# Optimization experiments

Hardware: AMD Instinct MI355X
Metric: run time of the kernel (lower is better)

Reference implementation:

```python
import jax, jax.numpy as jnp
import numpy as np

B, S, D, H, NUM_REL = 8, 1024, 1024, 16, 512
HD = D // H  # head size = 64


def setup_inputs() -> dict:
    key = jax.random.key(0)
    ks = jax.random.split(key, 12)
    sc = 0.02  # weight init scale for numerical stability
    inp = {
        "query": jax.random.normal(ks[0], (B, S, D), jnp.float32),
        "key": jax.random.normal(ks[1], (B, S, D), jnp.float32),
        "value": jax.random.normal(ks[2], (B, S, D), jnp.float32),
        "Wq": jax.random.normal(ks[3], (D, D), jnp.float32) * sc,
        "bq": jnp.zeros((D,), jnp.float32),
        "Wk": jax.random.normal(ks[4], (D, D), jnp.float32) * sc,
        "bk": jnp.zeros((D,), jnp.float32),
        "Wv": jax.random.normal(ks[5], (D, D), jnp.float32) * sc,
        "bv": jnp.zeros((D,), jnp.float32),
        "Wo": jax.random.normal(ks[6], (D, D), jnp.float32) * sc,
        "bo": jnp.zeros((D,), jnp.float32),
        "pos_table": jax.random.normal(ks[7], (NUM_REL, HD), jnp.float32) * sc,
        # True = masked position (causal: cannot attend to future)
        "mask": jnp.broadcast_to(jnp.triu(jnp.ones((S, S), bool), k=1), (B, S, S)),
    }
    return inp


def reference(query, key, value, Wq, bq, Wk, bk, Wv, bv, Wo, bo, pos_table, mask):
    Bq, Sq, Dm = query.shape
    hd = Dm // H

    def proj(x, W, b):
        # nn.Linear: x @ W.T + b, then split heads -> [B, H, S, hd]
        return (x @ W.T + b).reshape(Bq, Sq, H, hd).transpose(0, 2, 1, 3)

    q = proj(query, Wq, bq)
    k = proj(key, Wk, bk)
    v = proj(value, Wv, bv)

    scores = jnp.einsum("bhid,bhjd->bhij", q, k)

    # relative-position bias: idxs[i,j] = clip(i - j, 0, NUM_REL-1)
    t = jnp.arange(Sq)
    idxs = jnp.clip(t[:, None] - t[None, :], 0, pos_table.shape[0] - 1)
    pos = pos_table[idxs]  # [S, S, hd]
    scores = scores + jnp.einsum("bhid,ijd->bhij", q, pos)

    scores = scores / np.sqrt(hd).astype(np.float32)
    scores = jnp.where(mask[:, None, :, :], jnp.float32(-1e9), scores)
    prob = jax.nn.softmax(scores, axis=-1)  # dropout p=0.0 -> identity

    out = jnp.einsum("bhij,bhjd->bhid", prob, v)
    out = out.transpose(0, 2, 1, 3).reshape(Bq, Sq, Dm)
    return out @ Wo.T + bo
```

## Files before the change

kernel.cpp:

```cpp
#include <hip/hip_runtime.h>
#include <stdint.h>

#define DEV __device__ __forceinline__

typedef unsigned short u16;
typedef __bf16 bf16x8 __attribute__((ext_vector_type(8)));
typedef float  f32x4  __attribute__((ext_vector_type(4)));
typedef unsigned short u16x8 __attribute__((ext_vector_type(8)));
typedef unsigned short u16x4 __attribute__((ext_vector_type(4)));
typedef float  fvec4  __attribute__((ext_vector_type(4)));

constexpr int Sz   = 1024;
constexpr int Dm   = 1024;
constexpr int HDm  = 64;
constexpr int NREL = 512;
constexpr int Mrows = 8192;
constexpr int KV   = 32;

DEV u16 f2bf(float f) { return __builtin_bit_cast(u16, (__bf16)f); }
DEV float bf2f(u16 h) { return __builtin_bit_cast(float, (uint32_t)h << 16); }
DEV f32x4 mfma16(bf16x8 a, bf16x8 b, f32x4 c) {
  return __builtin_amdgcn_mfma_f32_16x16x32_bf16(a, b, c, 0, 0, 0);
}
DEV float ex2(float x) {
  float r;
  asm("v_exp_f32 %0, %1" : "=v"(r) : "v"(x));
  return r;
}

DEV u16x4 tr0(const u16* p) {
  u16x4 d;
  asm volatile("ds_read_b64_tr_b16 %0, %1"
               : "=v"(d)
               : "v"((const __attribute__((address_space(3))) u16*)p));
  return d;
}
DEV u16x4 tr512(const u16* p) {
  u16x4 d;
  asm volatile("ds_read_b64_tr_b16 %0, %1 offset:512"
               : "=v"(d)
               : "v"((const __attribute__((address_space(3))) u16*)p));
  return d;
}
DEV bf16x8 mk8(u16x4 a, u16x4 b) {
  u16x8 r;
  r[0] = a[0]; r[1] = a[1]; r[2] = a[2]; r[3] = a[3];
  r[4] = b[0]; r[5] = b[1]; r[6] = b[2]; r[7] = b[3];
  return __builtin_bit_cast(bf16x8, r);
}
DEV void gload(const u16* src, u16* dst) {
  __builtin_amdgcn_global_load_lds(
      (const __attribute__((address_space(1))) void*)src,
      (__attribute__((address_space(3))) void*)dst, 16, 0, 0);
}

__global__ __launch_bounds__(256) void cvt_kernel(const float* __restrict__ in,
                                                  u16* __restrict__ out) {
  size_t i = (size_t)blockIdx.x * 256 + threadIdx.x;
  fvec4 v = *(const fvec4*)(in + i * 4);
  u16x4 o;
  o[0] = f2bf(v[0]); o[1] = f2bf(v[1]); o[2] = f2bf(v[2]); o[3] = f2bf(v[3]);
  *(u16x4*)(out + i * 4) = o;
}

__global__ __launch_bounds__(256) void cvt3_kernel(const float* __restrict__ a,
                                                   const float* __restrict__ b,
                                                   const float* __restrict__ c,
                                                   u16* __restrict__ oa,
                                                   u16* __restrict__ ob,
                                                   u16* __restrict__ oc) {
  const int bid = blockIdx.x;
  const int seg = bid >> 13;
  const float* in = seg == 0 ? a : seg == 1 ? b : c;
  u16* out = seg == 0 ? oa : seg == 1 ? ob : oc;
  size_t i = (size_t)(bid & 8191) * 256 + threadIdx.x;
  fvec4 v = *(const fvec4*)(in + i * 4);
  u16x4 o;
  o[0] = f2bf(v[0]); o[1] = f2bf(v[1]); o[2] = f2bf(v[2]); o[3] = f2bf(v[3]);
  *(u16x4*)(out + i * 4) = o;
}

template<bool OUT_BF16>
DEV void gemm_body(const u16* __restrict__ A, const u16* __restrict__ Bw,
                   const float* __restrict__ bias, void* __restrict__ Cout,
                   int m0, int n0, u16* As, u16* Bs) {
  const int tid = threadIdx.x;
  const int wave = tid >> 6, lane = tid & 63;
  const int lr = lane & 15, lg = lane >> 4;
  const int wr = (wave >> 1) * 64, wc = (wave & 1) * 64;

  auto issue = [&](int t) {
    const int k0 = t * 64;
    u16* Ad = As + (t & 1) * (128 * 64);
    u16* Bd = Bs + (t & 1) * (128 * 64);
    #pragma unroll
    for (int it = 0; it < 4; ++it) {
      int chunk = it * 256 + tid;
      int row = chunk >> 3, c16 = chunk & 7;
      gload(Bw + (size_t)(n0 + row) * Dm + k0 + ((c16 ^ (row & 7)) * 8),
            Bd + (it * 256 + wave * 64) * 8);
      gload(A + (size_t)(m0 + row) * Dm + k0 + ((c16 ^ (row & 7)) * 8),
            Ad + (it * 256 + wave * 64) * 8);
    }
  };

  issue(0);
  f32x4 acc[4][4] = {};
  for (int t = 0; t < 16; ++t) {
    if (t < 15) {
      issue(t + 1);
      asm volatile("s_waitcnt vmcnt(8)" ::: "memory");
    } else {
      asm volatile("s_waitcnt vmcnt(0)" ::: "memory");
    }
    __builtin_amdgcn_s_barrier();
    const u16* Ab = As + (t & 1) * (128 * 64);
    const u16* Bb = Bs + (t & 1) * (128 * 64);
    #pragma unroll
    for (int kk = 0; kk < 2; ++kk) {
      bf16x8 af[4], bf_[4];
      #pragma unroll
      for (int m = 0; m < 4; ++m)
        af[m] = *(const bf16x8*)&Ab[(wr + m * 16 + lr) * 64 + (((kk * 4 + lg) ^ (lr & 7)) * 8)];
      #pragma unroll
      for (int n = 0; n < 4; ++n)
        bf_[n] = *(const bf16x8*)&Bb[(wc + n * 16 + lr) * 64 + (((kk * 4 + lg) ^ (lr & 7)) * 8)];
      __builtin_amdgcn_s_setprio(1);
      #pragma unroll
      for (int m = 0; m < 4; ++m)
        #pragma unroll
        for (int n = 0; n < 4; ++n)
          acc[m][n] = mfma16(af[m], bf_[n], acc[m][n]);
      __builtin_amdgcn_s_setprio(0);
    }
    __builtin_amdgcn_s_barrier();
  }

  float bv[4];
  #pragma unroll
  for (int n = 0; n < 4; ++n) bv[n] = bias[n0 + wc + n * 16 + lr];
  #pragma unroll
  for (int m = 0; m < 4; ++m) {
    #pragma unroll
    for (int n = 0; n < 4; ++n) {
      const int gcol = n0 + wc + n * 16 + lr;
      #pragma unroll
      for (int r = 0; r < 4; ++r) {
        const int grow = m0 + wr + m * 16 + lg * 4 + r;
        float v = acc[m][n][r] + bv[n];
        if (OUT_BF16)
          ((u16*)Cout)[(size_t)grow * Dm + gcol] = f2bf(v);
        else
          ((float*)Cout)[(size_t)grow * Dm + gcol] = v;
      }
    }
  }
}

template<bool OUT_BF16>
__global__ __launch_bounds__(256) void gemm1_kernel(const u16* __restrict__ A,
                                                    const u16* __restrict__ Bw,
                                                    const float* __restrict__ bias,
                                                    void* __restrict__ Cout) {
  __shared__ u16 As[2 * 128 * 64];
  __shared__ u16 Bs[2 * 128 * 64];
  const int r = blockIdx.x;
  const int xcd = r & 7, loc = r >> 3;
  const int m0 = (xcd * 8 + (loc & 7)) * 128;
  const int n0 = (loc >> 3) * 128;
  gemm_body<OUT_BF16>(A, Bw, bias, Cout, m0, n0, As, Bs);
}

__global__ __launch_bounds__(256) void gemm3_kernel(
    const u16* __restrict__ Xq, const u16* __restrict__ Xk, const u16* __restrict__ Xv,
    const u16* __restrict__ Wq, const u16* __restrict__ Wk, const u16* __restrict__ Wv,
    const float* __restrict__ bq, const float* __restrict__ bk, const float* __restrict__ bv,
    u16* __restrict__ Cq, u16* __restrict__ Ck, u16* __restrict__ Cv) {
  __shared__ u16 As[2 * 128 * 64];
  __shared__ u16 Bs[2 * 128 * 64];
  const int flat = blockIdx.x;
  const int seg = flat >> 9;
  const int r = flat & 511;
  const int xcd = r & 7, loc = r >> 3;
  const int m0 = (xcd * 8 + (loc & 7)) * 128;
  const int n0 = (loc >> 3) * 128;
  const u16* A = seg == 0 ? Xq : seg == 1 ? Xk : Xv;
  const u16* Bw = seg == 0 ? Wq : seg == 1 ? Wk : Wv;
  const float* bias = seg == 0 ? bq : seg == 1 ? bk : bv;
  u16* C = seg == 0 ? Cq : seg == 1 ? Ck : Cv;
  gemm_body<true>(A, Bw, bias, C, m0, n0, As, Bs);
}

__global__ __launch_bounds__(256, 4) void attn_kernel(const u16* __restrict__ Q,
                                                      const u16* __restrict__ Kb,
                                                      const u16* __restrict__ Vb,
                                                      const u16* __restrict__ posB,
                                                      u16* __restrict__ O) {
  __shared__ u16 Ks[2][KV * 64];
  __shared__ u16 Vs[2][KV * 64];
  __shared__ u16 ring[128 * 64];
  __shared__ u16 SH[4][16 * 40];

  const int tid = threadIdx.x;
  const int wave = tid >> 6, lane = tid & 63;
  const int lr = lane & 15, lg = lane >> 4;
  const int bid = blockIdx.x;
  const int xcd = bid & 7;
  const int idx = bid >> 3;
  const int bhl = idx & 15;
  const int pp_ = idx >> 4;
  const int bh  = xcd * 16 + bhl;
  const int b = bh >> 4, h = bh & 15;

  u16* SHW = SH[wave];
  const size_t rowbase = (size_t)(b * Sz) * Dm + h * HDm;

  const int krow = tid >> 3, kc = tid & 7;
  const int vj = ((tid >> 5) << 2) | ((tid >> 1) & 3);
  const int vd = ((tid >> 3) & 3) * 16 + (tid & 1) * 8;
  const int rrow = tid >> 3, rcol = tid & 7;

  auto issueKV = [&](int t) {
    const int j0 = t * KV;
    const int bsel = t & 1;
    gload(Kb + rowbase + (size_t)(j0 + krow) * Dm + ((kc ^ (krow & 7)) * 8),
          &Ks[bsel][wave * 512]);
    gload(Vb + rowbase + (size_t)(j0 + vj) * Dm + vd, &Vs[bsel][wave * 512]);
  };
  auto stageRing = [&](int cb) {
    const int rel = cb + rrow;
    const int slot = rel & 127;
    const int cl = rel < 0 ? 0 : (rel > NREL - 1 ? NREL - 1 : rel);
    gload(posB + cl * 64 + ((rcol ^ (slot & 7)) * 8),
          &ring[((cb & 127) + wave * 8) * 64]);
  };

  constexpr float SC = 0.125f * 1.44269504f;

  for (int job = 0; job < 2; ++job) {
    const int qi = job ? pp_ : 15 - pp_;
    const int qb = qi * 64;
    const int wq = qb + wave * 16;
    const int nt = 2 * qi + 2;
    const int qg = wq + lr;

    const u16* qptr = Q + rowbase + (size_t)(wq + lr) * Dm;
    bf16x8 qf[2];
    qf[0] = *(const bf16x8*)(qptr + lg * 8);
    qf[1] = *(const bf16x8*)(qptr + 32 + lg * 8);

    float b511;
    {
      const u16* pp = posB + (NREL - 1) * HDm;
      bf16x8 pa0 = *(const bf16x8*)(pp + lg * 8);
      bf16x8 pa1 = *(const bf16x8*)(pp + 32 + lg * 8);
      f32x4 a = {};
      a = mfma16(pa0, qf[0], a);
      a = mfma16(pa1, qf[1], a);
      b511 = a[0];
    }

    stageRing(qb + 32);
    stageRing(qb);
    stageRing(qb - 32);
    issueKV(0);

    f32x4 oacc[4] = {};
    float m_i = -1e30f, l_i = 0.f;

    for (int t = 0; t < nt; ++t) {
      const int j0 = t * KV;
      const int bsel = t & 1;
      const bool active = (j0 <= wq + 15);
      const bool clamp = (wq - j0 - 31) >= NREL - 1;
      const int wb = wq - j0 - 31;

      if (t + 1 < nt) {
        stageRing(qb - 32 * (t + 1) - 32);
        issueKV(t + 1);
        asm volatile("s_waitcnt vmcnt(3)" ::: "memory");
      } else {
        asm volatile("s_waitcnt vmcnt(0)" ::: "memory");
      }
      __builtin_amdgcn_s_barrier();

      if (active) {
        if (!clamp) {
          #pragma unroll
          for (int wg = 0; wg < 3; ++wg) {
            const int rrel = wb + wg * 16 + lr;
            const int slot = rrel & 127;
            const u16* rp = &ring[slot * 64];
            f32x4 a = {};
            a = mfma16(qf[0], *(const bf16x8*)&rp[((0 + lg) ^ (slot & 7)) * 8], a);
            a = mfma16(qf[1], *(const bf16x8*)&rp[((4 + lg) ^ (slot & 7)) * 8], a);
            #pragma unroll
            for (int r = 0; r < 4; ++r) {
              const int q = lg * 4 + r;
              const int col = q - (wg * 16 + lr) + 31;
              if (col >= 0 && col < 32)
                SHW[q * 40 + col] = f2bf(a[r]);
            }
          }
        }

        __builtin_amdgcn_s_setprio(1);
        f32x4 s0 = {}, s1 = {};
        const u16* KT = &Ks[bsel][0];
        s0 = mfma16(*(const bf16x8*)&KT[(0 + lr) * 64 + (((0 + lg) ^ (lr & 7)) * 8)], qf[0], s0);
        s0 = mfma16(*(const bf16x8*)&KT[(0 + lr) * 64 + (((4 + lg) ^ (lr & 7)) * 8)], qf[1], s0);
        s1 = mfma16(*(const bf16x8*)&KT[(16 + lr) * 64 + (((0 + lg) ^ (lr & 7)) * 8)], qf[0], s1);
        s1 = mfma16(*(const bf16x8*)&KT[(16 + lr) * 64 + (((4 + lg) ^ (lr & 7)) * 8)], qf[1], s1);
        __builtin_amdgcn_s_setprio(0);

        float p0[4], p1[4];
        float tmax = -3e38f;
        if (clamp) {
          #pragma unroll
          for (int r = 0; r < 4; ++r) {
            p0[r] = (s0[r] + b511) * SC; tmax = fmaxf(tmax, p0[r]);
            p1[r] = (s1[r] + b511) * SC; tmax = fmaxf(tmax, p1[r]);
          }
        } else {
          u16x4 bv0 = *(const u16x4*)&SHW[lr * 40 + lg * 4];
          u16x4 bv1 = *(const u16x4*)&SHW[lr * 40 + 16 + lg * 4];
          #pragma unroll
          for (int r = 0; r < 4; ++r) {
            float v0 = (s0[r] + bf2f(bv0[r])) * SC;
            if (j0 + lg * 4 + r > qg) v0 = -1e9f;
            p0[r] = v0; tmax = fmaxf(tmax, v0);
            float v1 = (s1[r] + bf2f(bv1[r])) * SC;
            if (j0 + 16 + lg * 4 + r > qg) v1 = -1e9f;
            p1[r] = v1; tmax = fmaxf(tmax, v1);
          }
        }
        tmax = fmaxf(tmax, __shfl_xor(tmax, 16));
        tmax = fmaxf(tmax, __shfl_xor(tmax, 32));

        if (!__all(tmax <= m_i + 11.5f)) {
          float mn = fmaxf(m_i, tmax);
          float sc = ex2(m_i - mn);
          m_i = mn; l_i *= sc;
          #pragma unroll
          for (int dg = 0; dg < 4; ++dg) oacc[dg] *= sc;
        }

        float lsum = 0.f;
        #pragma unroll
        for (int r = 0; r < 4; ++r) {
          p0[r] = ex2(p0[r] - m_i); lsum += p0[r];
          p1[r] = ex2(p1[r] - m_i); lsum += p1[r];
        }
        lsum += __shfl_xor(lsum, 16);
        lsum += __shfl_xor(lsum, 32);
        l_i += lsum;

        u16x4 pk0, pk1;
        #pragma unroll
        for (int r = 0; r < 4; ++r) { pk0[r] = f2bf(p0[r]); pk1[r] = f2bf(p1[r]); }
        *(u16x4*)&SHW[lr * 40 + lg * 4] = pk0;
        *(u16x4*)&SHW[lr * 40 + 16 + lg * 4] = pk1;

        bf16x8 pB = *(const bf16x8*)&SHW[lr * 40 + lg * 8];

        u16x4 va[4][2];
        #pragma unroll
        for (int dg = 0; dg < 4; ++dg) {
          const u16* base = &Vs[bsel][(2 * lg) * 256 + dg * 64 + lr * 4];
          va[dg][0] = tr0(base);
          va[dg][1] = tr512(base);
        }
        asm volatile("s_waitcnt lgkmcnt(0)" ::: "memory");
        __builtin_amdgcn_sched_barrier(0);
        __builtin_amdgcn_s_setprio(1);
        #pragma unroll
        for (int dg = 0; dg < 4; ++dg)
          oacc[dg] = mfma16(mk8(va[dg][0], va[dg][1]), pB, oacc[dg]);
        __builtin_amdgcn_s_setprio(0);
      }
      __builtin_amdgcn_s_barrier();
    }

    const float inv = 1.0f / l_i;
    const size_t obase = rowbase + (size_t)qg * Dm;
    #pragma unroll
    for (int dg = 0; dg < 4; ++dg) {
      u16x4 w;
      #pragma unroll
      for (int r = 0; r < 4; ++r) w[r] = f2bf(oacc[dg][r] * inv);
      *(u16x4*)&O[obase + dg * 16 + lg * 4] = w;
    }
  }
}

extern "C" void kernel_launch(void* const* d_in, const int* in_sizes, int n_in,
                              void* d_out, int out_size, void* d_ws, size_t ws_size,
                              hipStream_t stream) {
  const float* query = (const float*)d_in[0];
  const float* key   = (const float*)d_in[1];
  const float* value = (const float*)d_in[2];
  const float* Wq    = (const float*)d_in[3];
  const float* bq    = (const float*)d_in[4];
  const float* Wk    = (const float*)d_in[5];
  const float* bk    = (const float*)d_in[6];
  const float* Wv    = (const float*)d_in[7];
  const float* bv    = (const float*)d_in[8];
  const float* Wo    = (const float*)d_in[9];
  const float* bo    = (const float*)d_in[10];
  const float* pos   = (const float*)d_in[11];

  char* ws = (char*)d_ws;
  u16* WqB  = (u16*)(ws);
  u16* WkB  = (u16*)(ws + (2ull << 20));
  u16* WvB  = (u16*)(ws + (4ull << 20));
  u16* WoB  = (u16*)(ws + (6ull << 20));
  u16* posB = (u16*)(ws + (8ull << 20));
  u16* Xq   = (u16*)(ws + (9ull << 20));
  u16* Xk   = (u16*)(ws + (25ull << 20));
  u16* Xv   = (u16*)(ws + (41ull << 20));
  u16* Qb   = (u16*)(ws + (57ull << 20));
  u16* Kb   = (u16*)(ws + (73ull << 20));
  u16* Ob   = Xq;

  const bool bigws = ws_size >= (105ull << 20);
  u16* Vb = bigws ? (u16*)(ws + (89ull << 20)) : Xk;

  cvt_kernel<<<1024, 256, 0, stream>>>(Wq, WqB);
  cvt_kernel<<<1024, 256, 0, stream>>>(Wk, WkB);
  cvt_kernel<<<1024, 256, 0, stream>>>(Wv, WvB);
  cvt_kernel<<<1024, 256, 0, stream>>>(Wo, WoB);
  cvt_kernel<<<32,   256, 0, stream>>>(pos, posB);
  cvt3_kernel<<<24576, 256, 0, stream>>>(query, key, value, Xq, Xk, Xv);

  if (bigws) {
    gemm3_kernel<<<1536, 256, 0, stream>>>(Xq, Xk, Xv, WqB, WkB, WvB,
                                           bq, bk, bv, Qb, Kb, Vb);
  } else {
    gemm1_kernel<true><<<512, 256, 0, stream>>>(Xq, WqB, bq, Qb);
    gemm1_kernel<true><<<512, 256, 0, stream>>>(Xk, WkB, bk, Kb);
    gemm1_kernel<true><<<512, 256, 0, stream>>>(Xv, WvB, bv, Vb);
  }

  attn_kernel<<<1024, 256, 0, stream>>>(Qb, Kb, Vb, posB, Ob);

  gemm1_kernel<false><<<512, 256, 0, stream>>>(Ob, WoB, bo, d_out);
}
```

Measured before the change: 192.2 us.

## Fuse fp32-to-bf16 activation conversion into QKV GEMM and merge weight casts

The QKV projection GEMM now reads fp32 activations directly. It loads them into registers, converts them to bf16 and writes them to swizzled LDS, which removes the separate cvt3 pass that wrote and re-read 48MB of bf16 copies. The five small weight and pos-table conversion launches are merged into one kernel. The GEMM epilogue is changed to emit vectorized 4-wide stores by swapping the MFMA operand order, so each lane holds contiguous columns. In exchange, the fp32 A path waits on vmcnt(0) every iteration, and its register-staged prefetch may pipeline less deeply than the previous direct global-to-LDS double buffer.

```diff
diff --git a/kernel.cpp b/kernel.cpp
--- a/kernel.cpp
+++ b/kernel.cpp
@@ -54,36 +54,85 @@
       (__attribute__((address_space(3))) void*)dst, 16, 0, 0);
 }
 
-__global__ __launch_bounds__(256) void cvt_kernel(const float* __restrict__ in,
-                                                  u16* __restrict__ out) {
-  size_t i = (size_t)blockIdx.x * 256 + threadIdx.x;
+__global__ __launch_bounds__(256) void cvtw_kernel(const float* __restrict__ w0,
+                                                   const float* __restrict__ w1,
+                                                   const float* __restrict__ w2,
+                                                   const float* __restrict__ w3,
+                                                   const float* __restrict__ ps,
+                                                   u16* __restrict__ o0,
+                                                   u16* __restrict__ o1,
+                                                   u16* __restrict__ o2,
+                                                   u16* __restrict__ o3,
+                                                   u16* __restrict__ op) {
+  const int bid = blockIdx.x;
+  const float* in;
+  u16* out;
+  int local;
+  if (bid < 4096) {
+    const int s = bid >> 10;
+    in = s == 0 ? w0 : s == 1 ? w1 : s == 2 ? w2 : w3;
+    out = s == 0 ? o0 : s == 1 ? o1 : s == 2 ? o2 : o3;
+    local = bid & 1023;
+  } else {
+    in = ps; out = op; local = bid - 4096;
+  }
+  size_t i = (size_t)local * 256 + threadIdx.x;
   fvec4 v = *(const fvec4*)(in + i * 4);
   u16x4 o;
   o[0] = f2bf(v[0]); o[1] = f2bf(v[1]); o[2] = f2bf(v[2]); o[3] = f2bf(v[3]);
   *(u16x4*)(out + i * 4) = o;
 }
 
-__global__ __launch_bounds__(256) void cvt3_kernel(const float* __restrict__ a,
-                                                   const float* __restrict__ b,
-                                                   const float* __restrict__ c,
-                                                   u16* __restrict__ oa,
-                                                   u16* __restrict__ ob,
-                                                   u16* __restrict__ oc) {
-  const int bid = blockIdx.x;
-  const int seg = bid >> 13;
-  const float* in = seg == 0 ? a : seg == 1 ? b : c;
-  u16* out = seg == 0 ? oa : seg == 1 ? ob : oc;
-  size_t i = (size_t)(bid & 8191) * 256 + threadIdx.x;
-  fvec4 v = *(const fvec4*)(in + i * 4);
-  u16x4 o;
-  o[0] = f2bf(v[0]); o[1] = f2bf(v[1]); o[2] = f2bf(v[2]); o[3] = f2bf(v[3]);
-  *(u16x4*)(out + i * 4) = o;
-}
-
 template<bool OUT_BF16>
-DEV void gemm_body(const u16* __restrict__ A, const u16* __restrict__ Bw,
-                   const float* __restrict__ bias, void* __restrict__ Cout,
-                   int m0, int n0, u16* As, u16* Bs) {
+DEV void gemm_epilogue(const float* bias, void* Cout, int m0, int n0,
+                       int wr, int wc, int lr, int lg, f32x4 acc[4][4]) {
+  #pragma unroll
+  for (int m = 0; m < 4; ++m) {
+    const int grow = m0 + wr + m * 16 + lr;
+    #pragma unroll
+    for (int n = 0; n < 4; ++n) {
+      const int gcol = n0 + wc + n * 16 + lg * 4;
+      fvec4 bb = *(const fvec4*)&bias[gcol];
+      if (OUT_BF16) {
+        u16x4 w;
+        #pragma unroll
+        for (int r = 0; r < 4; ++r) w[r] = f2bf(acc[m][n][r] + bb[r]);
+        *(u16x4*)&((u16*)Cout)[(size_t)grow * Dm + gcol] = w;
+      } else {
+        fvec4 w;
+        #pragma unroll
+        for (int r = 0; r < 4; ++r) w[r] = acc[m][n][r] + bb[r];
+        *(fvec4*)&((float*)Cout)[(size_t)grow * Dm + gcol] = w;
+      }
+    }
+  }
+}
+
+DEV void gemm_compute(const u16* Ab, const u16* Bb, int wr, int wc,
+                      int lr, int lg, f32x4 acc[4][4]) {
+  #pragma unroll
+  for (int kk = 0; kk < 2; ++kk) {
+    bf16x8 af[4], bf_[4];
+    #pragma unroll
+    for (int m = 0; m < 4; ++m)
+      af[m] = *(const bf16x8*)&Ab[(wr + m * 16 + lr) * 64 + (((kk * 4 + lg) ^ (lr & 7)) * 8)];
+    #pragma unroll
+    for (int n = 0; n < 4; ++n)
+      bf_[n] = *(const bf16x8*)&Bb[(wc + n * 16 + lr) * 64 + (((kk * 4 + lg) ^ (lr & 7)) * 8)];
+    __builtin_amdgcn_s_setprio(1);
+    #pragma unroll
+    for (int m = 0; m < 4; ++m)
+      #pragma unroll
+      for (int n = 0; n < 4; ++n)
+        acc[m][n] = mfma16(bf_[n], af[m], acc[m][n]);
+    __builtin_amdgcn_s_setprio(0);
+  }
+}
+
+template<bool OUT_BF16>
+DEV void gemm_body16(const u16* __restrict__ A, const u16* __restrict__ Bw,
+                     const float* __restrict__ bias, void* __restrict__ Cout,
+                     int m0, int n0, u16* As, u16* Bs) {
   const int tid = threadIdx.x;
   const int wave = tid >> 6, lane = tid & 63;
   const int lr = lane & 15, lg = lane >> 4;
@@ -114,47 +163,70 @@
       asm volatile("s_waitcnt vmcnt(0)" ::: "memory");
     }
     __builtin_amdgcn_s_barrier();
-    const u16* Ab = As + (t & 1) * (128 * 64);
-    const u16* Bb = Bs + (t & 1) * (128 * 64);
-    #pragma unroll
-    for (int kk = 0; kk < 2; ++kk) {
-      bf16x8 af[4], bf_[4];
-      #pragma unroll
-      for (int m = 0; m < 4; ++m)
-        af[m] = *(const bf16x8*)&Ab[(wr + m * 16 + lr) * 64 + (((kk * 4 + lg) ^ (lr & 7)) * 8)];
-      #pragma unroll
-      for (int n = 0; n < 4; ++n)
-        bf_[n] = *(const bf16x8*)&Bb[(wc + n * 16 + lr) * 64 + (((kk * 4 + lg) ^ (lr & 7)) * 8)];
-      __builtin_amdgcn_s_setprio(1);
-      #pragma unroll
-      for (int m = 0; m < 4; ++m)
-        #pragma unroll
-        for (int n = 0; n < 4; ++n)
-          acc[m][n] = mfma16(af[m], bf_[n], acc[m][n]);
-      __builtin_amdgcn_s_setprio(0);
-    }
+    gemm_compute(As + (t & 1) * (128 * 64), Bs + (t & 1) * (128 * 64),
+                 wr, wc, lr, lg, acc);
     __builtin_amdgcn_s_barrier();
   }
-
-  float bv[4];
-  #pragma unroll
-  for (int n = 0; n < 4; ++n) bv[n] = bias[n0 + wc + n * 16 + lr];
-  #pragma unroll
-  for (int m = 0; m < 4; ++m) {
-    #pragma unroll
-    for (int n = 0; n < 4; ++n) {
-      const int gcol = n0 + wc + n * 16 + lr;
+  gemm_epilogue<OUT_BF16>(bias, Cout, m0, n0, wr, wc, lr, lg, acc);
+}
+
+template<bool OUT_BF16>
+DEV void gemm_body32(const float* __restrict__ A, const u16* __restrict__ Bw,
+                     const float* __restrict__ bias, void* __restrict__ Cout,
+                     int m0, int n0, u16* As, u16* Bs) {
+  const int tid = threadIdx.x;
+  const int wave = tid >> 6, lane = tid & 63;
+  const int lr = lane & 15, lg = lane >> 4;
+  const int wr = (wave >> 1) * 64, wc = (wave & 1) * 64;
+  const int row = tid >> 3 << 2, c16 = tid & 7;
+
+  auto issueB = [&](int t) {
+    const int k0 = t * 64;
+    u16* Bd = Bs + (t & 1) * (128 * 64);
+    #pragma unroll
+    for (int it = 0; it < 4; ++it) {
+      int chunk = it * 256 + tid;
+      int rw = chunk >> 3, cc = chunk & 7;
+      gload(Bw + (size_t)(n0 + rw) * Dm + k0 + ((cc ^ (rw & 7)) * 8),
+            Bd + (it * 256 + wave * 64) * 8);
+    }
+  };
+
+  fvec4 ar[4][2];
+  auto loadA = [&](int t) {
+    const int k0 = t * 64;
+    #pragma unroll
+    for (int it = 0; it < 4; ++it) {
+      int chunk = it * 256 + tid;
+      int rw = chunk >> 3, cc = chunk & 7;
+      const float* src = A + (size_t)(m0 + rw) * Dm + k0 + cc * 8;
+      ar[it][0] = *(const fvec4*)src;
+      ar[it][1] = *(const fvec4*)(src + 4);
+    }
+  };
+
+  issueB(0);
+  loadA(0);
+  f32x4 acc[4][4] = {};
+  for (int t = 0; t < 16; ++t) {
+    asm volatile("s_waitcnt vmcnt(0)" ::: "memory");
+    u16* Ad = As + (t & 1) * (128 * 64);
+    #pragma unroll
+    for (int it = 0; it < 4; ++it) {
+      int chunk = it * 256 + tid;
+      int rw = chunk >> 3, cc = chunk & 7;
+      u16x8 v;
       #pragma unroll
-      for (int r = 0; r < 4; ++r) {
-        const int grow = m0 + wr + m * 16 + lg * 4 + r;
-        float v = acc[m][n][r] + bv[n];
-        if (OUT_BF16)
-          ((u16*)Cout)[(size_t)grow * Dm + gcol] = f2bf(v);
-        else
-          ((float*)Cout)[(size_t)grow * Dm + gcol] = v;
-      }
-    }
+      for (int e = 0; e < 4; ++e) { v[e] = f2bf(ar[it][0][e]); v[e + 4] = f2bf(ar[it][1][e]); }
+      *(u16x8*)&Ad[rw * 64 + ((cc ^ (rw & 7)) * 8)] = v;
+    }
+    if (t < 15) { issueB(t + 1); loadA(t + 1); }
+    asm volatile("s_waitcnt lgkmcnt(0)" ::: "memory");
+    __builtin_amdgcn_s_barrier();
+    gemm_compute(Ad, Bs + (t & 1) * (128 * 64), wr, wc, lr, lg, acc);
+    __builtin_amdgcn_s_barrier();
   }
+  gemm_epilogue<OUT_BF16>(bias, Cout, m0, n0, wr, wc, lr, lg, acc);
 }
 
 template<bool OUT_BF16>
@@ -168,11 +240,11 @@
   const int xcd = r & 7, loc = r >> 3;
   const int m0 = (xcd * 8 + (loc & 7)) * 128;
   const int n0 = (loc >> 3) * 128;
-  gemm_body<OUT_BF16>(A, Bw, bias, Cout, m0, n0, As, Bs);
+  gemm_body16<OUT_BF16>(A, Bw, bias, Cout, m0, n0, As, Bs);
 }
 
 __global__ __launch_bounds__(256) void gemm3_kernel(
-    const u16* __restrict__ Xq, const u16* __restrict__ Xk, const u16* __restrict__ Xv,
+    const float* __restrict__ Xq, const float* __restrict__ Xk, const float* __restrict__ Xv,
     const u16* __restrict__ Wq, const u16* __restrict__ Wk, const u16* __restrict__ Wv,
     const float* __restrict__ bq, const float* __restrict__ bk, const float* __restrict__ bv,
     u16* __restrict__ Cq, u16* __restrict__ Ck, u16* __restrict__ Cv) {
@@ -184,11 +256,11 @@
   const int xcd = r & 7, loc = r >> 3;
   const int m0 = (xcd * 8 + (loc & 7)) * 128;
   const int n0 = (loc >> 3) * 128;
-  const u16* A = seg == 0 ? Xq : seg == 1 ? Xk : Xv;
+  const float* A = seg == 0 ? Xq : seg == 1 ? Xk : Xv;
   const u16* Bw = seg == 0 ? Wq : seg == 1 ? Wk : Wv;
   const float* bias = seg == 0 ? bq : seg == 1 ? bk : bv;
   u16* C = seg == 0 ? Cq : seg == 1 ? Ck : Cv;
-  gemm_body<true>(A, Bw, bias, C, m0, n0, As, Bs);
+  gemm_body32<true>(A, Bw, bias, C, m0, n0, As, Bs);
 }
 
 __global__ __launch_bounds__(256, 4) void attn_kernel(const u16* __restrict__ Q,
@@ -415,31 +487,16 @@
   u16* WvB  = (u16*)(ws + (4ull << 20));
   u16* WoB  = (u16*)(ws + (6ull << 20));
   u16* posB = (u16*)(ws + (8ull << 20));
-  u16* Xq   = (u16*)(ws + (9ull << 20));
-  u16* Xk   = (u16*)(ws + (25ull << 20));
-  u16* Xv   = (u16*)(ws + (41ull << 20));
-  u16* Qb   = (u16*)(ws + (57ull << 20));
-  u16* Kb   = (u16*)(ws + (73ull << 20));
-  u16* Ob   = Xq;
-
-  const bool bigws = ws_size >= (105ull << 20);
-  u16* Vb = bigws ? (u16*)(ws + (89ull << 20)) : Xk;
-
-  cvt_kernel<<<1024, 256, 0, stream>>>(Wq, WqB);
-  cvt_kernel<<<1024, 256, 0, stream>>>(Wk, WkB);
-  cvt_kernel<<<1024, 256, 0, stream>>>(Wv, WvB);
-  cvt_kernel<<<1024, 256, 0, stream>>>(Wo, WoB);
-  cvt_kernel<<<32,   256, 0, stream>>>(pos, posB);
-  cvt3_kernel<<<24576, 256, 0, stream>>>(query, key, value, Xq, Xk, Xv);
-
-  if (bigws) {
-    gemm3_kernel<<<1536, 256, 0, stream>>>(Xq, Xk, Xv, WqB, WkB, WvB,
-                                           bq, bk, bv, Qb, Kb, Vb);
-  } else {
-    gemm1_kernel<true><<<512, 256, 0, stream>>>(Xq, WqB, bq, Qb);
-    gemm1_kernel<true><<<512, 256, 0, stream>>>(Xk, WkB, bk, Kb);
-    gemm1_kernel<true><<<512, 256, 0, stream>>>(Xv, WvB, bv, Vb);
-  }
+  u16* Qb   = (u16*)(ws + (9ull << 20));
+  u16* Kb   = (u16*)(ws + (25ull << 20));
+  u16* Vb   = (u16*)(ws + (41ull << 20));
+  u16* Ob   = (u16*)(ws + (57ull << 20));
+
+  cvtw_kernel<<<4128, 256, 0, stream>>>(Wq, Wk, Wv, Wo, pos,
+                                        WqB, WkB, WvB, WoB, posB);
+
+  gemm3_kernel<<<1536, 256, 0, stream>>>(query, key, value, WqB, WkB, WvB,
+                                         bq, bk, bv, Qb, Kb, Vb);
 
   attn_kernel<<<1024, 256, 0, stream>>>(Qb, Kb, Vb, posB, Ob);
 
```

Result: faster. 185.0 us (-3.7%).
